# Optimization experiments

Measured on AMD Instinct MI355X. Metric: run time of the kernel, lower is better.

The kernel has to match this reference:

```python
import jax, jax.numpy as jnp
import numpy as np

N = 100000      # nodes
E = 1600000     # edges
NW = 512        # num_words (input feature dim)
H = 128         # hidden_size
L = 3           # num_layers
G = 256         # num graphs
NEG = 0.2       # GAT leaky_relu slope
EPS = 1e-5      # batchnorm eps


def setup_inputs() -> dict:
    key = jax.random.key(0)
    ks = jax.random.split(key, 20)
    x = jax.random.normal(ks[0], (N, NW), jnp.float32)
    edge_index = jax.random.randint(ks[1], (2, E), 0, N, dtype=jnp.int64)
    edge_attr = jax.random.randint(ks[2], (E,), 0, 8, dtype=jnp.int64)
    batch = jnp.sort(jax.random.randint(ks[3], (N,), 0, G, dtype=jnp.int64))
    edge_emb = jax.random.normal(ks[4], (8, H), jnp.float32) * 0.05
    W0 = jax.random.normal(ks[5], (NW, H), jnp.float32) / np.sqrt(NW)
    W_rest = jax.random.normal(ks[6], (L - 1, H, H), jnp.float32) / np.sqrt(H)
    att_src = jax.random.normal(ks[7], (L, H), jnp.float32) / np.sqrt(H)
    att_dst = jax.random.normal(ks[8], (L, H), jnp.float32) / np.sqrt(H)
    bias = jax.random.normal(ks[9], (L, H), jnp.float32) * 0.02
    gamma = 1.0 + jax.random.normal(ks[10], (L, H), jnp.float32) * 0.1
    beta = jax.random.normal(ks[11], (L, H), jnp.float32) * 0.02
    gate_w1 = jax.random.normal(ks[12], (H, H), jnp.float32) / np.sqrt(H)
    gate_b1 = jnp.zeros((H,), jnp.float32)
    gate_w2 = jax.random.normal(ks[13], (H, 1), jnp.float32) / np.sqrt(H)
    gate_b2 = jnp.zeros((1,), jnp.float32)
    cls_w = jax.random.normal(ks[14], (H, 2), jnp.float32) / np.sqrt(H)
    cls_b = jnp.zeros((2,), jnp.float32)
    return {"x": x, "edge_index": edge_index, "edge_attr": edge_attr, "batch": batch,
            "edge_emb": edge_emb, "W0": W0, "W_rest": W_rest, "att_src": att_src,
            "att_dst": att_dst, "bias": bias, "gamma": gamma, "beta": beta,
            "gate_w1": gate_w1, "gate_b1": gate_b1, "gate_w2": gate_w2,
            "gate_b2": gate_b2, "cls_w": cls_w, "cls_b": cls_b}


def _gat_layer(x, W, a_s, a_d, b, src, dst):
    # PyG GATConv, heads=1, concat=True: h = xW; e_ij = leaky(a_s.h_src + a_d.h_dst)
    h = x @ W                                   # [N, H]
    a_src = h @ a_s                             # [N]
    a_dst = h @ a_d                             # [N]
    e = jax.nn.leaky_relu(a_src[src] + a_dst[dst], NEG)      # [E+N]
    m = jax.ops.segment_max(e, dst, num_segments=N)          # scatter-softmax over dst
    ex = jnp.exp(e - m[dst])
    den = jax.ops.segment_sum(ex, dst, num_segments=N)
    coef = ex / den[dst]                                      # [E+N]
    out = jax.ops.segment_sum(h[src] * coef[:, None], dst, num_segments=N)
    return out + b


def _batchnorm_relu(x, g, bt):
    mu = jnp.mean(x, axis=0)
    var = jnp.mean((x - mu) ** 2, axis=0)      # biased variance (torch BN forward)
    return jax.nn.relu((x - mu) * jax.lax.rsqrt(var + EPS) * g + bt)


def reference(x, edge_index, edge_attr, batch, edge_emb, W0, W_rest, att_src,
              att_dst, bias, gamma, beta, gate_w1, gate_b1, gate_w2, gate_b2,
              cls_w, cls_b):
    _ = edge_emb[edge_attr]  # computed in original module but never used (DCE'd)
    # add self-loops as GATConv does by default
    loop = jnp.arange(N, dtype=edge_index.dtype)
    src = jnp.concatenate([edge_index[0], loop])
    dst = jnp.concatenate([edge_index[1], loop])
    Ws = [W0] + [W_rest[i] for i in range(L - 1)]
    for i in range(L):
        x = _gat_layer(x, Ws[i], att_src[i], att_dst[i], bias[i], src, dst)
        x = _batchnorm_relu(x, gamma[i], beta[i])  # dropout is identity in eval
    # GlobalAttention pooling: gate = MLP(x) -> segment softmax over graphs
    gate = jax.nn.relu(x @ gate_w1 + gate_b1) @ gate_w2 + gate_b2   # [N, 1]
    gate = gate[:, 0]
    gm = jax.ops.segment_max(gate, batch, num_segments=G)
    gex = jnp.exp(gate - gm[batch])
    gden = jax.ops.segment_sum(gex, batch, num_segments=G)
    gden = jnp.where(gden == 0, 1.0, gden)
    coef = gex / gden[batch]
    pooled = jax.ops.segment_sum(x * coef[:, None], batch, num_segments=G)  # [G, H]
    logits = pooled @ cls_w + cls_b
    return jax.nn.log_softmax(logits, axis=-1)
```

## Files before the change

kernel.cpp:

```cpp
#include <hip/hip_runtime.h>

#define kN  100000
#define kE  1600000
#define kNW 512
#define kH  128
#define kL  3
#define kG  256
#define kNEG 0.2f
#define kEPS 1e-5f

typedef __attribute__((ext_vector_type(8))) short bf16x8;
typedef __attribute__((ext_vector_type(4))) float f32x4;

static __device__ __forceinline__ float lrelu(float v) { return v >= 0.f ? v : kNEG * v; }

static __device__ __forceinline__ unsigned short bf16rn(float x) {
    unsigned u = __float_as_uint(x);
    return (unsigned short)((u + 0x7FFFu + ((u >> 16) & 1u)) >> 16);
}
static __device__ __forceinline__ float bf16tof(unsigned short h) {
    return __uint_as_float(((unsigned)h) << 16);
}

__global__ void count_deg(const int* __restrict__ ei, int* __restrict__ deg, int E) {
    int e = blockIdx.x * 256 + threadIdx.x;
    if (e < E) atomicAdd(&deg[ei[E + e]], 1);
}

__global__ void scan1(const int* __restrict__ deg, int* __restrict__ bsums, int n) {
    __shared__ int sdata[256];
    int b = blockIdx.x, t = threadIdx.x;
    int base = b * 1024 + t * 4;
    int s = 0;
#pragma unroll
    for (int j = 0; j < 4; j++) { int i = base + j; s += (i < n) ? deg[i] : 0; }
    sdata[t] = s; __syncthreads();
    for (int st = 128; st > 0; st >>= 1) { if (t < st) sdata[t] += sdata[t + st]; __syncthreads(); }
    if (t == 0) bsums[b] = sdata[0];
}

__global__ void scan2(int* __restrict__ bsums, int nb, int* __restrict__ row_ptr_last) {
    __shared__ int lds[128];
    int t = threadIdx.x;
    int v = (t < nb) ? bsums[t] : 0;
    lds[t] = v; __syncthreads();
    for (int st = 1; st < 128; st <<= 1) {
        int x = 0;
        if (t >= st) x = lds[t - st];
        __syncthreads();
        if (t >= st) lds[t] += x;
        __syncthreads();
    }
    if (t < nb) bsums[t] = lds[t] - v;
    if (t == nb - 1) row_ptr_last[0] = lds[t];
}

__global__ void scan3(const int* __restrict__ deg, const int* __restrict__ bsums,
                      int* __restrict__ row_ptr, int* __restrict__ cursor, int n) {
    __shared__ int lds[256];
    int b = blockIdx.x, t = threadIdx.x;
    int base = b * 1024 + t * 4;
    int v[4]; int s = 0;
#pragma unroll
    for (int j = 0; j < 4; j++) { int i = base + j; v[j] = (i < n) ? deg[i] : 0; s += v[j]; }
    lds[t] = s; __syncthreads();
    for (int st = 1; st < 256; st <<= 1) {
        int x = 0;
        if (t >= st) x = lds[t - st];
        __syncthreads();
        if (t >= st) lds[t] += x;
        __syncthreads();
    }
    int excl = (t == 0) ? 0 : lds[t - 1];
    excl += bsums[b];
    int run = excl;
#pragma unroll
    for (int j = 0; j < 4; j++) {
        int i = base + j;
        if (i < n) { row_ptr[i] = run; cursor[i] = run; run += v[j]; }
    }
}

__global__ void fill_csr(const int* __restrict__ ei, int* __restrict__ cursor,
                         int* __restrict__ col_src, int E) {
    int e = blockIdx.x * 256 + threadIdx.x;
    if (e < E) {
        int s = ei[e], d = ei[E + e];
        int p = atomicAdd(&cursor[d], 1);
        col_src[p] = s;
    }
}

__global__ void pack_a(const float* __restrict__ A, unsigned short* __restrict__ apk,
                       int Kpitch, int kbase, int NKT) {
    int g = blockIdx.x * 256 + threadIdx.x;
    int lane = g & 63;
    int t2 = g >> 6;
    int kt = t2 % NKT;
    int rt = t2 / NKT;
    int row = rt * 16 + (lane & 15);
    int k0 = kbase + kt * 32 + (lane >> 4) * 8;
    const float* src = A + (size_t)row * Kpitch + k0;
    float4 v0 = *(const float4*)src;
    float4 v1 = *(const float4*)(src + 4);
    float v[8] = {v0.x, v0.y, v0.z, v0.w, v1.x, v1.y, v1.z, v1.w};
    unsigned short h[8], l[8];
#pragma unroll
    for (int j = 0; j < 8; j++) {
        h[j] = bf16rn(v[j]);
        l[j] = bf16rn(v[j] - bf16tof(h[j]));
    }
    size_t slot = ((size_t)(rt * NKT + kt) * 2) * 512 + lane * 8;
    int4 vhi = make_int4((unsigned)h[0] | ((unsigned)h[1] << 16), (unsigned)h[2] | ((unsigned)h[3] << 16),
                         (unsigned)h[4] | ((unsigned)h[5] << 16), (unsigned)h[6] | ((unsigned)h[7] << 16));
    int4 vlo = make_int4((unsigned)l[0] | ((unsigned)l[1] << 16), (unsigned)l[2] | ((unsigned)l[3] << 16),
                         (unsigned)l[4] | ((unsigned)l[5] << 16), (unsigned)l[6] | ((unsigned)l[7] << 16));
    *(int4*)(apk + slot) = vhi;
    *(int4*)(apk + slot + 512) = vlo;
}

__global__ void pack_b_all(const float* __restrict__ W0, const float* __restrict__ Wr,
                           const float* __restrict__ Gw1,
                           unsigned short* __restrict__ b0a, unsigned short* __restrict__ b0b,
                           unsigned short* __restrict__ b1, unsigned short* __restrict__ b2,
                           unsigned short* __restrict__ bg) {
    int bid = blockIdx.x;
    const float* src; unsigned short* dst; int kbase; int NKT; int lb;
    if (bid < 16)      { src = W0;            dst = b0a; kbase = 0;   NKT = 8; lb = bid; }
    else if (bid < 32) { src = W0;            dst = b0b; kbase = 256; NKT = 8; lb = bid - 16; }
    else if (bid < 40) { src = Wr;            dst = b1;  kbase = 0;   NKT = 4; lb = bid - 32; }
    else if (bid < 48) { src = Wr + 128*128;  dst = b2;  kbase = 0;   NKT = 4; lb = bid - 40; }
    else               { src = Gw1;           dst = bg;  kbase = 0;   NKT = 4; lb = bid - 48; }
    int g = lb * 256 + threadIdx.x;
    int lane = g & 63;
    int t2 = g >> 6;
    int kt = t2 % NKT;
    int ct = t2 / NKT;
    int col = ct * 16 + (lane & 15);
    int k0 = kbase + kt * 32 + (lane >> 4) * 8;
    unsigned short h[8], l[8];
#pragma unroll
    for (int j = 0; j < 8; j++) {
        float v = src[(size_t)(k0 + j) * 128 + col];
        h[j] = bf16rn(v);
        l[j] = bf16rn(v - bf16tof(h[j]));
    }
    size_t slot = ((size_t)(ct * NKT + kt) * 2) * 512 + lane * 8;
    int4 vhi = make_int4((unsigned)h[0] | ((unsigned)h[1] << 16), (unsigned)h[2] | ((unsigned)h[3] << 16),
                         (unsigned)h[4] | ((unsigned)h[5] << 16), (unsigned)h[6] | ((unsigned)h[7] << 16));
    int4 vlo = make_int4((unsigned)l[0] | ((unsigned)l[1] << 16), (unsigned)l[2] | ((unsigned)l[3] << 16),
                         (unsigned)l[4] | ((unsigned)l[5] << 16), (unsigned)l[6] | ((unsigned)l[7] << 16));
    *(int4*)(dst + slot) = vhi;
    *(int4*)(dst + slot + 512) = vlo;
}

__global__ __launch_bounds__(256) void gemm_mfma(const unsigned short* __restrict__ apk,
                                                 const unsigned short* __restrict__ bpk,
                                                 float* __restrict__ C, int M, int NKT,
                                                 int accum, const float* __restrict__ bias,
                                                 int do_relu) {
    int tid = threadIdx.x;
    int w = tid >> 6, lane = tid & 63;
    int rt0 = blockIdx.x * 8 + (w >> 1) * 4;
    int ct0 = (w & 1) * 4;
    int laneoff = lane * 8;
    f32x4 acc[4][4];
#pragma unroll
    for (int i = 0; i < 4; i++)
#pragma unroll
        for (int j = 0; j < 4; j++) acc[i][j] = (f32x4){0.f, 0.f, 0.f, 0.f};

    for (int kt = 0; kt < NKT; ++kt) {
        bf16x8 Ah[4], Al[4], Bh[4], Bl[4];
#pragma unroll
        for (int f = 0; f < 4; f++) {
            size_t ao = ((size_t)((rt0 + f) * NKT + kt) * 2) * 512 + laneoff;
            Ah[f] = *(const bf16x8*)(apk + ao);
            Al[f] = *(const bf16x8*)(apk + ao + 512);
            size_t bo = ((size_t)((ct0 + f) * NKT + kt) * 2) * 512 + laneoff;
            Bh[f] = *(const bf16x8*)(bpk + bo);
            Bl[f] = *(const bf16x8*)(bpk + bo + 512);
        }
#pragma unroll
        for (int i = 0; i < 4; i++)
#pragma unroll
            for (int j = 0; j < 4; j++) {
                acc[i][j] = __builtin_amdgcn_mfma_f32_16x16x32_bf16(Ah[i], Bh[j], acc[i][j], 0, 0, 0);
                acc[i][j] = __builtin_amdgcn_mfma_f32_16x16x32_bf16(Ah[i], Bl[j], acc[i][j], 0, 0, 0);
                acc[i][j] = __builtin_amdgcn_mfma_f32_16x16x32_bf16(Al[i], Bh[j], acc[i][j], 0, 0, 0);
            }
    }
    int cbase = ct0 * 16 + (lane & 15);
    int rgrp = (lane >> 4) * 4;
#pragma unroll
    for (int i = 0; i < 4; i++) {
        int rbase = (rt0 + i) * 16 + rgrp;
#pragma unroll
        for (int j = 0; j < 4; j++) {
            int col = cbase + j * 16;
#pragma unroll
            for (int r = 0; r < 4; r++) {
                int row = rbase + r;
                if (row < M) {
                    float v = acc[i][j][r];
                    if (accum) v += C[(size_t)row * 128 + col];
                    if (bias) v += bias[col];
                    if (do_relu) v = fmaxf(v, 0.f);
                    C[(size_t)row * 128 + col] = v;
                }
            }
        }
    }
}

__global__ void att_dots(const float* __restrict__ h, const float* __restrict__ ws_,
                         const float* __restrict__ wd_, float* __restrict__ a_s,
                         float* __restrict__ a_d, int n) {
    int v = blockIdx.x * 4 + (threadIdx.x >> 6);
    int lane = threadIdx.x & 63;
    if (v >= n) return;
    float2 hx = ((const float2*)(h + (size_t)v * 128))[lane];
    float2 ws = ((const float2*)ws_)[lane];
    float2 wd = ((const float2*)wd_)[lane];
    float ps = hx.x * ws.x + hx.y * ws.y;
    float pd = hx.x * wd.x + hx.y * wd.y;
#pragma unroll
    for (int off = 32; off; off >>= 1) {
        ps += __shfl_xor(ps, off);
        pd += __shfl_xor(pd, off);
    }
    if (lane == 0) { a_s[v] = ps; a_d[v] = pd; }
}

__global__ void edge_softmax(const int* __restrict__ row_ptr, const int* __restrict__ col_src,
                             const float* __restrict__ a_s, const float* __restrict__ a_d,
                             float* __restrict__ coef, float* __restrict__ coef_self, int n) {
    int v = blockIdx.x * 4 + (threadIdx.x >> 6);
    int lane = threadIdx.x & 63;
    if (v >= n) return;
    int s0 = row_ptr[v], s1 = row_ptr[v + 1];
    float adv = a_d[v];
    float es = lrelu(a_s[v] + adv);
    float mx = es;
    for (int k = s0 + lane; k < s1; k += 64) {
        float e = lrelu(a_s[col_src[k]] + adv);
        coef[k] = e;
        mx = fmaxf(mx, e);
    }
#pragma unroll
    for (int off = 32; off; off >>= 1) mx = fmaxf(mx, __shfl_xor(mx, off));
    float sum = 0.f;
    for (int k = s0 + lane; k < s1; k += 64) {
        float ex = expf(coef[k] - mx);
        coef[k] = ex;
        sum += ex;
    }
    if (lane == 0) sum += expf(es - mx);
#pragma unroll
    for (int off = 32; off; off >>= 1) sum += __shfl_xor(sum, off);
    float inv = 1.f / sum;
    for (int k = s0 + lane; k < s1; k += 64) coef[k] *= inv;
    if (lane == 0) coef_self[v] = expf(es - mx) * inv;
}

__global__ void aggregate(const int* __restrict__ row_ptr, const int* __restrict__ col_src,
                          const float* __restrict__ coef, const float* __restrict__ coef_self,
                          const float* __restrict__ h, const float* __restrict__ bias,
                          float* __restrict__ out, int n) {
    int v = blockIdx.x * 4 + (threadIdx.x >> 6);
    int lane = threadIdx.x & 63;
    if (v >= n) return;
    int s0 = row_ptr[v], s1 = row_ptr[v + 1];
    const float2* h2 = (const float2*)h;
    float cs = coef_self[v];
    float2 hv = h2[(size_t)v * 64 + lane];
    float ax = cs * hv.x, ay = cs * hv.y;
    for (int k = s0; k < s1; k++) {
        int s = col_src[k];
        float c = coef[k];
        float2 hs = h2[(size_t)s * 64 + lane];
        ax += c * hs.x;
        ay += c * hs.y;
    }
    float2 b = ((const float2*)bias)[lane];
    float2 o; o.x = ax + b.x; o.y = ay + b.y;
    ((float2*)out)[(size_t)v * 64 + lane] = o;
}

__global__ void bn_stats(const float* __restrict__ x, double* __restrict__ sums, int n) {
    int col = threadIdx.x & 127;
    int half = threadIdx.x >> 7;
    double s = 0.0, q = 0.0;
    for (int r = blockIdx.x * 2 + half; r < n; r += gridDim.x * 2) {
        float v = x[(size_t)r * 128 + col];
        s += v;
        q += (double)v * (double)v;
    }
    __shared__ double ls[256], lq[256];
    ls[threadIdx.x] = s; lq[threadIdx.x] = q;
    __syncthreads();
    if (half == 0) {
        s += ls[threadIdx.x + 128];
        q += lq[threadIdx.x + 128];
        atomicAdd(&sums[col], s);
        atomicAdd(&sums[128 + col], q);
    }
}

__global__ void bn_finalize(const double* __restrict__ sums, const float* __restrict__ gamma,
                            const float* __restrict__ beta, float* __restrict__ coefs, int n) {
    int c = threadIdx.x;
    if (c < 128) {
        double mu = sums[c] / n;
        double var = sums[128 + c] / n - mu * mu;
        double rs = 1.0 / sqrt(var + (double)kEPS);
        float sc = (float)rs * gamma[c];
        coefs[c] = sc;
        coefs[128 + c] = beta[c] - (float)(mu * rs) * gamma[c];
    }
}

__global__ void bn_apply_pack(const float* __restrict__ xin, const float* __restrict__ coefs,
                              unsigned short* __restrict__ apk, float* __restrict__ xout, int n) {
    int idx = blockIdx.x * 256 + threadIdx.x;
    if (idx >= n * 32) return;
    float4 v = ((const float4*)xin)[idx];
    int c4 = idx & 31;
    int r = idx >> 5;
    int c = c4 * 4;
    v.x = fmaxf(v.x * coefs[c + 0] + coefs[128 + c + 0], 0.f);
    v.y = fmaxf(v.y * coefs[c + 1] + coefs[128 + c + 1], 0.f);
    v.z = fmaxf(v.z * coefs[c + 2] + coefs[128 + c + 2], 0.f);
    v.w = fmaxf(v.w * coefs[c + 3] + coefs[128 + c + 3], 0.f);
    if (xout) ((float4*)xout)[idx] = v;
    int rt = r >> 4;
    int kt = c >> 5;
    int lane = (r & 15) + (((c >> 3) & 3) << 4);
    int half = c4 & 1;
    size_t slot = ((size_t)(rt * 4 + kt) * 2) * 512 + lane * 8 + half * 4;
    float vv[4] = {v.x, v.y, v.z, v.w};
    unsigned short h[4], l[4];
#pragma unroll
    for (int j = 0; j < 4; j++) {
        h[j] = bf16rn(vv[j]);
        l[j] = bf16rn(vv[j] - bf16tof(h[j]));
    }
    int2 vhi = make_int2((unsigned)h[0] | ((unsigned)h[1] << 16), (unsigned)h[2] | ((unsigned)h[3] << 16));
    int2 vlo = make_int2((unsigned)l[0] | ((unsigned)l[1] << 16), (unsigned)l[2] | ((unsigned)l[3] << 16));
    *(int2*)(apk + slot) = vhi;
    *(int2*)(apk + slot + 512) = vlo;
}

__global__ void gate_dot(const float* __restrict__ hidden, const float* __restrict__ gw2,
                         const float* __restrict__ gb2, float* __restrict__ gate, int n) {
    int v = blockIdx.x * 4 + (threadIdx.x >> 6);
    int lane = threadIdx.x & 63;
    if (v >= n) return;
    float2 hx = ((const float2*)(hidden + (size_t)v * 128))[lane];
    float2 w = ((const float2*)gw2)[lane];
    float p = hx.x * w.x + hx.y * w.y;
#pragma unroll
    for (int off = 32; off; off >>= 1) p += __shfl_xor(p, off);
    if (lane == 0) gate[v] = p + gb2[0];
}

__global__ void graph_bounds(const int* __restrict__ batch, int* __restrict__ gstart, int n, int g) {
    int i = blockIdx.x * 256 + threadIdx.x;
    if (i > g) return;
    int lo = 0, hi = n;
    while (lo < hi) {
        int mid = (lo + hi) >> 1;
        if (batch[mid] < i) lo = mid + 1; else hi = mid;
    }
    gstart[i] = lo;
}

__global__ __launch_bounds__(512) void pool(const float* __restrict__ x, const float* __restrict__ gate,
                                            const int* __restrict__ gstart, float* __restrict__ pooled) {
    int g = blockIdx.x;
    int t = threadIdx.x;
    int col = t & 127;
    int q = t >> 7;
    int s0 = gstart[g], s1 = gstart[g + 1];
    __shared__ float red[8];
    __shared__ float acc_lds[512];
    float mx = -INFINITY;
    for (int v = s0 + t; v < s1; v += 512) mx = fmaxf(mx, gate[v]);
#pragma unroll
    for (int off = 32; off; off >>= 1) mx = fmaxf(mx, __shfl_xor(mx, off));
    if ((t & 63) == 0) red[t >> 6] = mx;
    __syncthreads();
    mx = fmaxf(fmaxf(fmaxf(red[0], red[1]), fmaxf(red[2], red[3])),
               fmaxf(fmaxf(red[4], red[5]), fmaxf(red[6], red[7])));
    __syncthreads();
    float sum = 0.f;
    for (int v = s0 + t; v < s1; v += 512) sum += expf(gate[v] - mx);
#pragma unroll
    for (int off = 32; off; off >>= 1) sum += __shfl_xor(sum, off);
    if ((t & 63) == 0) red[t >> 6] = sum;
    __syncthreads();
    sum = red[0] + red[1] + red[2] + red[3] + red[4] + red[5] + red[6] + red[7];
    if (sum == 0.f) sum = 1.f;
    float inv = 1.f / sum;
    float acc = 0.f;
    for (int v = s0 + q; v < s1; v += 4) {
        float c = expf(gate[v] - mx) * inv;
        acc += x[(size_t)v * 128 + col] * c;
    }
    acc_lds[t] = acc;
    __syncthreads();
    if (q == 0)
        pooled[(size_t)g * 128 + col] = acc_lds[col] + acc_lds[128 + col] +
                                        acc_lds[256 + col] + acc_lds[384 + col];
}

__global__ void classify(const float* __restrict__ pooled, const float* __restrict__ cls_w,
                         const float* __restrict__ cls_b, float* __restrict__ out, int g_) {
    int g = blockIdx.x * 4 + (threadIdx.x >> 6);
    int lane = threadIdx.x & 63;
    if (g >= g_) return;
    float2 p = ((const float2*)(pooled + (size_t)g * 128))[lane];
    float4 w = ((const float4*)cls_w)[lane];
    float l0 = p.x * w.x + p.y * w.z;
    float l1 = p.x * w.y + p.y * w.w;
#pragma unroll
    for (int off = 32; off; off >>= 1) {
        l0 += __shfl_xor(l0, off);
        l1 += __shfl_xor(l1, off);
    }
    if (lane == 0) {
        l0 += cls_b[0]; l1 += cls_b[1];
        float m = fmaxf(l0, l1);
        float lse = m + logf(expf(l0 - m) + expf(l1 - m));
        out[g * 2 + 0] = l0 - lse;
        out[g * 2 + 1] = l1 - lse;
    }
}

extern "C" void kernel_launch(void* const* d_in, const int* in_sizes, int n_in,
                              void* d_out, int out_size, void* d_ws, size_t ws_size,
                              hipStream_t stream) {
    const float* x        = (const float*)d_in[0];
    const int*   ei       = (const int*)d_in[1];
    const int*   batch    = (const int*)d_in[3];
    const float* W0       = (const float*)d_in[5];
    const float* W_rest   = (const float*)d_in[6];
    const float* att_src  = (const float*)d_in[7];
    const float* att_dst  = (const float*)d_in[8];
    const float* bias     = (const float*)d_in[9];
    const float* gamma    = (const float*)d_in[10];
    const float* beta     = (const float*)d_in[11];
    const float* gate_w1  = (const float*)d_in[12];
    const float* gate_b1  = (const float*)d_in[13];
    const float* gate_w2  = (const float*)d_in[14];
    const float* gate_b2  = (const float*)d_in[15];
    const float* cls_w    = (const float*)d_in[16];
    const float* cls_b    = (const float*)d_in[17];
    float* out = (float*)d_out;

    char* ws = (char*)d_ws;
    size_t off = 0;
    auto take = [&](size_t bytes) -> void* {
        void* p = ws + off;
        off += (bytes + 255) & ~(size_t)255;
        return p;
    };
    const int NRT = 6256;
    float* h         = (float*)take((size_t)kN * kH * 4);
    float* xa        = (float*)take((size_t)kN * kH * 4);
    unsigned short* apk = (unsigned short*)take((size_t)NRT * 8 * 2 * 512 * 2);
    unsigned short* bpk0a = (unsigned short*)take(8 * 8 * 2 * 512 * 2);
    unsigned short* bpk0b = (unsigned short*)take(8 * 8 * 2 * 512 * 2);
    unsigned short* bpk1  = (unsigned short*)take(8 * 4 * 2 * 512 * 2);
    unsigned short* bpk2  = (unsigned short*)take(8 * 4 * 2 * 512 * 2);
    unsigned short* bpkg  = (unsigned short*)take(8 * 4 * 2 * 512 * 2);
    float* a_s       = (float*)take((size_t)kN * 4);
    float* a_d       = (float*)take((size_t)kN * 4);
    float* coef_self = (float*)take((size_t)kN * 4);
    int*   deg       = (int*)take((size_t)kN * 4);
    int*   cursor    = (int*)take((size_t)kN * 4);
    int*   row_ptr   = (int*)take((size_t)(kN + 1) * 4);
    int*   col_src   = (int*)take((size_t)kE * 4);
    float* coef_csr  = (float*)take((size_t)kE * 4);
    int*   bsums     = (int*)take(1024 * 4);
    double* bn_sums  = (double*)take(256 * 8);
    float* bn_coefs  = (float*)take(256 * 4);
    float* gate      = (float*)take((size_t)kN * 4);
    int*   gstart    = (int*)take((size_t)(kG + 1) * 4);
    float* pooled    = (float*)take((size_t)kG * kH * 4);
    (void)ws_size; (void)in_sizes; (void)n_in; (void)out_size;

    const int NB = (kN + 1023) / 1024;
    const int GEMM_BLKS = (kN + 127) / 128;

    hipMemsetAsync(deg, 0, (size_t)kN * 4, stream);
    count_deg<<<(kE + 255) / 256, 256, 0, stream>>>(ei, deg, kE);
    scan1<<<NB, 256, 0, stream>>>(deg, bsums, kN);
    scan2<<<1, 128, 0, stream>>>(bsums, NB, row_ptr + kN);
    scan3<<<NB, 256, 0, stream>>>(deg, bsums, row_ptr, cursor, kN);
    fill_csr<<<(kE + 255) / 256, 256, 0, stream>>>(ei, cursor, col_src, kE);

    pack_b_all<<<56, 256, 0, stream>>>(W0, W_rest, gate_w1, bpk0a, bpk0b, bpk1, bpk2, bpkg);

    pack_a<<<6250 * 8 / 4, 256, 0, stream>>>(x, apk, kNW, 0, 8);
    gemm_mfma<<<GEMM_BLKS, 256, 0, stream>>>(apk, bpk0a, h, kN, 8, 0, nullptr, 0);
    pack_a<<<6250 * 8 / 4, 256, 0, stream>>>(x, apk, kNW, 256, 8);
    gemm_mfma<<<GEMM_BLKS, 256, 0, stream>>>(apk, bpk0b, h, kN, 8, 1, nullptr, 0);

    for (int l = 0; l < kL; l++) {
        if (l > 0) {
            const unsigned short* bp = (l == 1) ? bpk1 : bpk2;
            gemm_mfma<<<GEMM_BLKS, 256, 0, stream>>>(apk, bp, h, kN, 4, 0, nullptr, 0);
        }
        att_dots<<<(kN + 3) / 4, 256, 0, stream>>>(h, att_src + (size_t)l * kH,
                                                   att_dst + (size_t)l * kH, a_s, a_d, kN);
        edge_softmax<<<(kN + 3) / 4, 256, 0, stream>>>(row_ptr, col_src, a_s, a_d,
                                                       coef_csr, coef_self, kN);
        aggregate<<<(kN + 3) / 4, 256, 0, stream>>>(row_ptr, col_src, coef_csr, coef_self,
                                                    h, bias + (size_t)l * kH, xa, kN);
        hipMemsetAsync(bn_sums, 0, 256 * 8, stream);
        bn_stats<<<1024, 256, 0, stream>>>(xa, bn_sums, kN);
        bn_finalize<<<1, 128, 0, stream>>>(bn_sums, gamma + (size_t)l * kH,
                                           beta + (size_t)l * kH, bn_coefs, kN);
        bn_apply_pack<<<((kN * 32) + 255) / 256, 256, 0, stream>>>(
            xa, bn_coefs, apk, (l == kL - 1) ? xa : nullptr, kN);
    }

    gemm_mfma<<<GEMM_BLKS, 256, 0, stream>>>(apk, bpkg, h, kN, 4, 0, gate_b1, 1);
    gate_dot<<<(kN + 3) / 4, 256, 0, stream>>>(h, gate_w2, gate_b2, gate, kN);

    graph_bounds<<<2, 256, 0, stream>>>(batch, gstart, kN, kG);
    pool<<<kG, 512, 0, stream>>>(xa, gate, gstart, pooled);
    classify<<<(kG + 3) / 4, 256, 0, stream>>>(pooled, cls_w, cls_b, out, kG);
}
```

Measured before the change: 1.613 ms.

## Fuse packing, batchnorm-apply and attention dots into GEMM; fuse edge softmax with aggregation

The GEMM now reads fp32 activations directly and splits them into bf16 hi/lo inside the kernel. It applies the previous layer's batchnorm+ReLU in its prologue and computes the attention (or gate) dot products in its epilogue. This removes the separate pack_a, bn_apply_pack, att_dots and gate_dot passes and their intermediate buffers. Edge softmax and neighbor aggregation are merged into one kernel that builds exp weights on the fly, avoiding the E-sized coefficient array, and bn_stats is vectorized. The trade-off is heavier GEMM kernels with redundant per-tile conversion, possible register pressure, and dropping gate_b2, which relies on softmax shift invariance.

```diff
diff --git a/kernel.cpp b/kernel.cpp
--- a/kernel.cpp
+++ b/kernel.cpp
@@ -91,53 +91,23 @@
     }
 }
 
-__global__ void pack_a(const float* __restrict__ A, unsigned short* __restrict__ apk,
-                       int Kpitch, int kbase, int NKT) {
-    int g = blockIdx.x * 256 + threadIdx.x;
-    int lane = g & 63;
-    int t2 = g >> 6;
-    int kt = t2 % NKT;
-    int rt = t2 / NKT;
-    int row = rt * 16 + (lane & 15);
-    int k0 = kbase + kt * 32 + (lane >> 4) * 8;
-    const float* src = A + (size_t)row * Kpitch + k0;
-    float4 v0 = *(const float4*)src;
-    float4 v1 = *(const float4*)(src + 4);
-    float v[8] = {v0.x, v0.y, v0.z, v0.w, v1.x, v1.y, v1.z, v1.w};
-    unsigned short h[8], l[8];
-#pragma unroll
-    for (int j = 0; j < 8; j++) {
-        h[j] = bf16rn(v[j]);
-        l[j] = bf16rn(v[j] - bf16tof(h[j]));
-    }
-    size_t slot = ((size_t)(rt * NKT + kt) * 2) * 512 + lane * 8;
-    int4 vhi = make_int4((unsigned)h[0] | ((unsigned)h[1] << 16), (unsigned)h[2] | ((unsigned)h[3] << 16),
-                         (unsigned)h[4] | ((unsigned)h[5] << 16), (unsigned)h[6] | ((unsigned)h[7] << 16));
-    int4 vlo = make_int4((unsigned)l[0] | ((unsigned)l[1] << 16), (unsigned)l[2] | ((unsigned)l[3] << 16),
-                         (unsigned)l[4] | ((unsigned)l[5] << 16), (unsigned)l[6] | ((unsigned)l[7] << 16));
-    *(int4*)(apk + slot) = vhi;
-    *(int4*)(apk + slot + 512) = vlo;
-}
-
 __global__ void pack_b_all(const float* __restrict__ W0, const float* __restrict__ Wr,
                            const float* __restrict__ Gw1,
-                           unsigned short* __restrict__ b0a, unsigned short* __restrict__ b0b,
-                           unsigned short* __restrict__ b1, unsigned short* __restrict__ b2,
-                           unsigned short* __restrict__ bg) {
+                           unsigned short* __restrict__ b0, unsigned short* __restrict__ b1,
+                           unsigned short* __restrict__ b2, unsigned short* __restrict__ bg) {
     int bid = blockIdx.x;
-    const float* src; unsigned short* dst; int kbase; int NKT; int lb;
-    if (bid < 16)      { src = W0;            dst = b0a; kbase = 0;   NKT = 8; lb = bid; }
-    else if (bid < 32) { src = W0;            dst = b0b; kbase = 256; NKT = 8; lb = bid - 16; }
-    else if (bid < 40) { src = Wr;            dst = b1;  kbase = 0;   NKT = 4; lb = bid - 32; }
-    else if (bid < 48) { src = Wr + 128*128;  dst = b2;  kbase = 0;   NKT = 4; lb = bid - 40; }
-    else               { src = Gw1;           dst = bg;  kbase = 0;   NKT = 4; lb = bid - 48; }
+    const float* src; unsigned short* dst; int NKT; int lb;
+    if (bid < 32)      { src = W0;            dst = b0; NKT = 16; lb = bid; }
+    else if (bid < 40) { src = Wr;            dst = b1; NKT = 4;  lb = bid - 32; }
+    else if (bid < 48) { src = Wr + 128*128;  dst = b2; NKT = 4;  lb = bid - 40; }
+    else               { src = Gw1;           dst = bg; NKT = 4;  lb = bid - 48; }
     int g = lb * 256 + threadIdx.x;
     int lane = g & 63;
     int t2 = g >> 6;
     int kt = t2 % NKT;
     int ct = t2 / NKT;
     int col = ct * 16 + (lane & 15);
-    int k0 = kbase + kt * 32 + (lane >> 4) * 8;
+    int k0 = kt * 32 + (lane >> 4) * 8;
     unsigned short h[8], l[8];
 #pragma unroll
     for (int j = 0; j < 8; j++) {
@@ -154,16 +124,28 @@
     *(int4*)(dst + slot + 512) = vlo;
 }
 
-__global__ __launch_bounds__(256) void gemm_mfma(const unsigned short* __restrict__ apk,
-                                                 const unsigned short* __restrict__ bpk,
-                                                 float* __restrict__ C, int M, int NKT,
-                                                 int accum, const float* __restrict__ bias,
-                                                 int do_relu) {
+__global__ __launch_bounds__(256) void gemm_cvt(const float* __restrict__ A, int Kpitch, int NKT,
+                                                const unsigned short* __restrict__ bpk,
+                                                float* __restrict__ C, int M,
+                                                const float* __restrict__ bias, int do_relu,
+                                                const float* __restrict__ abn,
+                                                const float* __restrict__ att_s,
+                                                const float* __restrict__ att_d,
+                                                float* __restrict__ a_s, float* __restrict__ a_d) {
+    __shared__ float sAs[4][64], sAd[4][64];
     int tid = threadIdx.x;
     int w = tid >> 6, lane = tid & 63;
     int rt0 = blockIdx.x * 8 + (w >> 1) * 4;
     int ct0 = (w & 1) * 4;
     int laneoff = lane * 8;
+    int ksub = (lane >> 4) * 8;
+    const float* arow[4];
+#pragma unroll
+    for (int f = 0; f < 4; f++) {
+        int row = (rt0 + f) * 16 + (lane & 15);
+        if (row > M - 1) row = M - 1;
+        arow[f] = A + (size_t)row * Kpitch;
+    }
     f32x4 acc[4][4];
 #pragma unroll
     for (int i = 0; i < 4; i++)
@@ -171,12 +153,32 @@
         for (int j = 0; j < 4; j++) acc[i][j] = (f32x4){0.f, 0.f, 0.f, 0.f};
 
     for (int kt = 0; kt < NKT; ++kt) {
+        int k0 = kt * 32 + ksub;
+        float sc[8], sh[8];
+        if (abn) {
+            float4 s0 = *(const float4*)(abn + k0);
+            float4 s1 = *(const float4*)(abn + k0 + 4);
+            float4 t0 = *(const float4*)(abn + 128 + k0);
+            float4 t1 = *(const float4*)(abn + 128 + k0 + 4);
+            sc[0]=s0.x; sc[1]=s0.y; sc[2]=s0.z; sc[3]=s0.w;
+            sc[4]=s1.x; sc[5]=s1.y; sc[6]=s1.z; sc[7]=s1.w;
+            sh[0]=t0.x; sh[1]=t0.y; sh[2]=t0.z; sh[3]=t0.w;
+            sh[4]=t1.x; sh[5]=t1.y; sh[6]=t1.z; sh[7]=t1.w;
+        }
         bf16x8 Ah[4], Al[4], Bh[4], Bl[4];
 #pragma unroll
         for (int f = 0; f < 4; f++) {
-            size_t ao = ((size_t)((rt0 + f) * NKT + kt) * 2) * 512 + laneoff;
-            Ah[f] = *(const bf16x8*)(apk + ao);
-            Al[f] = *(const bf16x8*)(apk + ao + 512);
+            float4 v0 = *(const float4*)(arow[f] + k0);
+            float4 v1 = *(const float4*)(arow[f] + k0 + 4);
+            float v[8] = {v0.x, v0.y, v0.z, v0.w, v1.x, v1.y, v1.z, v1.w};
+#pragma unroll
+            for (int j = 0; j < 8; j++) {
+                float vj = v[j];
+                if (abn) vj = fmaxf(vj * sc[j] + sh[j], 0.f);
+                unsigned short hh = bf16rn(vj);
+                Ah[f][j] = (short)hh;
+                Al[f][j] = (short)bf16rn(vj - bf16tof(hh));
+            }
             size_t bo = ((size_t)((ct0 + f) * NKT + kt) * 2) * 512 + laneoff;
             Bh[f] = *(const bf16x8*)(bpk + bo);
             Bl[f] = *(const bf16x8*)(bpk + bo + 512);
@@ -192,122 +194,174 @@
     }
     int cbase = ct0 * 16 + (lane & 15);
     int rgrp = (lane >> 4) * 4;
+    float atts[4], attd[4];
+    if (att_s) {
+#pragma unroll
+        for (int j = 0; j < 4; j++) { atts[j] = att_s[cbase + j * 16]; attd[j] = att_d[cbase + j * 16]; }
+    }
+    float asp[4][4], adp[4][4];
 #pragma unroll
     for (int i = 0; i < 4; i++) {
         int rbase = (rt0 + i) * 16 + rgrp;
 #pragma unroll
+        for (int r = 0; r < 4; r++) { asp[i][r] = 0.f; adp[i][r] = 0.f; }
+#pragma unroll
         for (int j = 0; j < 4; j++) {
             int col = cbase + j * 16;
 #pragma unroll
             for (int r = 0; r < 4; r++) {
+                float val = acc[i][j][r];
+                if (bias) val += bias[col];
+                if (do_relu) val = fmaxf(val, 0.f);
                 int row = rbase + r;
-                if (row < M) {
-                    float v = acc[i][j][r];
-                    if (accum) v += C[(size_t)row * 128 + col];
-                    if (bias) v += bias[col];
-                    if (do_relu) v = fmaxf(v, 0.f);
-                    C[(size_t)row * 128 + col] = v;
+                if (C && row < M) C[(size_t)row * 128 + col] = val;
+                if (att_s) { asp[i][r] += val * atts[j]; adp[i][r] += val * attd[j]; }
+            }
+        }
+    }
+    if (att_s) {
+#pragma unroll
+        for (int i = 0; i < 4; i++)
+#pragma unroll
+            for (int r = 0; r < 4; r++) {
+                float s = asp[i][r], d = adp[i][r];
+#pragma unroll
+                for (int off = 1; off < 16; off <<= 1) {
+                    s += __shfl_xor(s, off);
+                    d += __shfl_xor(d, off);
+                }
+                if ((lane & 15) == 0) {
+                    int rl = i * 16 + rgrp + r;
+                    sAs[w][rl] = s; sAd[w][rl] = d;
                 }
             }
+        __syncthreads();
+        if (tid < 128) {
+            int grow = blockIdx.x * 128 + tid;
+            if (grow < M) {
+                int wp = (tid >> 6) * 2, rl = tid & 63;
+                a_s[grow] = sAs[wp][rl] + sAs[wp + 1][rl];
+                if (a_d) a_d[grow] = sAd[wp][rl] + sAd[wp + 1][rl];
+            }
         }
     }
 }
 
-__global__ void att_dots(const float* __restrict__ h, const float* __restrict__ ws_,
-                         const float* __restrict__ wd_, float* __restrict__ a_s,
-                         float* __restrict__ a_d, int n) {
-    int v = blockIdx.x * 4 + (threadIdx.x >> 6);
-    int lane = threadIdx.x & 63;
-    if (v >= n) return;
-    float2 hx = ((const float2*)(h + (size_t)v * 128))[lane];
-    float2 ws = ((const float2*)ws_)[lane];
-    float2 wd = ((const float2*)wd_)[lane];
-    float ps = hx.x * ws.x + hx.y * ws.y;
-    float pd = hx.x * wd.x + hx.y * wd.y;
-#pragma unroll
-    for (int off = 32; off; off >>= 1) {
-        ps += __shfl_xor(ps, off);
-        pd += __shfl_xor(pd, off);
-    }
-    if (lane == 0) { a_s[v] = ps; a_d[v] = pd; }
-}
-
-__global__ void edge_softmax(const int* __restrict__ row_ptr, const int* __restrict__ col_src,
-                             const float* __restrict__ a_s, const float* __restrict__ a_d,
-                             float* __restrict__ coef, float* __restrict__ coef_self, int n) {
+static __device__ __forceinline__ void gather_chunk(const float2* __restrict__ h2, int lane,
+                                                    int s_l, float ex_l, int cnt,
+                                                    float& ax, float& ay) {
+    for (int e0 = 0; e0 < cnt; e0 += 8) {
+        int t0 = __shfl(s_l, e0 + 0); float c0 = __shfl(ex_l, e0 + 0);
+        int t1 = __shfl(s_l, e0 + 1); float c1 = __shfl(ex_l, e0 + 1);
+        int t2 = __shfl(s_l, e0 + 2); float c2 = __shfl(ex_l, e0 + 2);
+        int t3 = __shfl(s_l, e0 + 3); float c3 = __shfl(ex_l, e0 + 3);
+        int t4 = __shfl(s_l, e0 + 4); float c4 = __shfl(ex_l, e0 + 4);
+        int t5 = __shfl(s_l, e0 + 5); float c5 = __shfl(ex_l, e0 + 5);
+        int t6 = __shfl(s_l, e0 + 6); float c6 = __shfl(ex_l, e0 + 6);
+        int t7 = __shfl(s_l, e0 + 7); float c7 = __shfl(ex_l, e0 + 7);
+        float2 h0 = h2[(size_t)t0 * 64 + lane];
+        float2 h1 = h2[(size_t)t1 * 64 + lane];
+        float2 h2v = h2[(size_t)t2 * 64 + lane];
+        float2 h3 = h2[(size_t)t3 * 64 + lane];
+        float2 h4 = h2[(size_t)t4 * 64 + lane];
+        float2 h5 = h2[(size_t)t5 * 64 + lane];
+        float2 h6 = h2[(size_t)t6 * 64 + lane];
+        float2 h7 = h2[(size_t)t7 * 64 + lane];
+        ax += c0 * h0.x + c1 * h1.x + c2 * h2v.x + c3 * h3.x
+            + c4 * h4.x + c5 * h5.x + c6 * h6.x + c7 * h7.x;
+        ay += c0 * h0.y + c1 * h1.y + c2 * h2v.y + c3 * h3.y
+            + c4 * h4.y + c5 * h5.y + c6 * h6.y + c7 * h7.y;
+    }
+}
+
+__global__ __launch_bounds__(256) void gat_edge(const int* __restrict__ row_ptr,
+                                                const int* __restrict__ col_src,
+                                                const float* __restrict__ a_s,
+                                                const float* __restrict__ a_d,
+                                                const float* __restrict__ h,
+                                                const float* __restrict__ bias,
+                                                float* __restrict__ out, int n) {
     int v = blockIdx.x * 4 + (threadIdx.x >> 6);
     int lane = threadIdx.x & 63;
     if (v >= n) return;
     int s0 = row_ptr[v], s1 = row_ptr[v + 1];
     float adv = a_d[v];
-    float es = lrelu(a_s[v] + adv);
-    float mx = es;
-    for (int k = s0 + lane; k < s1; k += 64) {
-        float e = lrelu(a_s[col_src[k]] + adv);
-        coef[k] = e;
-        mx = fmaxf(mx, e);
-    }
+    float e_self = lrelu(a_s[v] + adv);
+    int idx0 = s0 + lane;
+    bool act0 = idx0 < s1;
+    int sl0 = act0 ? col_src[idx0] : 0;
+    float el0 = act0 ? lrelu(a_s[sl0] + adv) : -1e30f;
+    float mx = fmaxf(e_self, el0);
+    for (int k = s0 + 64 + lane; k < s1; k += 64)
+        mx = fmaxf(mx, lrelu(a_s[col_src[k]] + adv));
 #pragma unroll
     for (int off = 32; off; off >>= 1) mx = fmaxf(mx, __shfl_xor(mx, off));
-    float sum = 0.f;
-    for (int k = s0 + lane; k < s1; k += 64) {
-        float ex = expf(coef[k] - mx);
-        coef[k] = ex;
-        sum += ex;
-    }
-    if (lane == 0) sum += expf(es - mx);
-#pragma unroll
-    for (int off = 32; off; off >>= 1) sum += __shfl_xor(sum, off);
-    float inv = 1.f / sum;
-    for (int k = s0 + lane; k < s1; k += 64) coef[k] *= inv;
-    if (lane == 0) coef_self[v] = expf(es - mx) * inv;
-}
-
-__global__ void aggregate(const int* __restrict__ row_ptr, const int* __restrict__ col_src,
-                          const float* __restrict__ coef, const float* __restrict__ coef_self,
-                          const float* __restrict__ h, const float* __restrict__ bias,
-                          float* __restrict__ out, int n) {
-    int v = blockIdx.x * 4 + (threadIdx.x >> 6);
-    int lane = threadIdx.x & 63;
-    if (v >= n) return;
-    int s0 = row_ptr[v], s1 = row_ptr[v + 1];
+
     const float2* h2 = (const float2*)h;
-    float cs = coef_self[v];
+    float ax = 0.f, ay = 0.f, den = 0.f;
+    {
+        float exl = act0 ? __expf(el0 - mx) : 0.f;
+        den += exl;
+        int cnt = s1 - s0; if (cnt > 64) cnt = 64;
+        gather_chunk(h2, lane, sl0, exl, cnt, ax, ay);
+    }
+    for (int k0 = s0 + 64; k0 < s1; k0 += 64) {
+        int idx = k0 + lane;
+        bool act = idx < s1;
+        int s_l = act ? col_src[idx] : 0;
+        float exl = act ? __expf(lrelu(a_s[s_l] + adv) - mx) : 0.f;
+        den += exl;
+        int cnt = s1 - k0; if (cnt > 64) cnt = 64;
+        gather_chunk(h2, lane, s_l, exl, cnt, ax, ay);
+    }
+#pragma unroll
+    for (int off = 32; off; off >>= 1) den += __shfl_xor(den, off);
+    float es = __expf(e_self - mx);
+    den += es;
     float2 hv = h2[(size_t)v * 64 + lane];
-    float ax = cs * hv.x, ay = cs * hv.y;
-    for (int k = s0; k < s1; k++) {
-        int s = col_src[k];
-        float c = coef[k];
-        float2 hs = h2[(size_t)s * 64 + lane];
-        ax += c * hs.x;
-        ay += c * hs.y;
-    }
+    ax += es * hv.x; ay += es * hv.y;
+    float inv = 1.f / den;
     float2 b = ((const float2*)bias)[lane];
-    float2 o; o.x = ax + b.x; o.y = ay + b.y;
+    float2 o; o.x = ax * inv + b.x; o.y = ay * inv + b.y;
     ((float2*)out)[(size_t)v * 64 + lane] = o;
 }
 
-__global__ void bn_stats(const float* __restrict__ x, double* __restrict__ sums, int n) {
-    int col = threadIdx.x & 127;
-    int half = threadIdx.x >> 7;
-    double s = 0.0, q = 0.0;
-    for (int r = blockIdx.x * 2 + half; r < n; r += gridDim.x * 2) {
-        float v = x[(size_t)r * 128 + col];
-        s += v;
-        q += (double)v * (double)v;
-    }
-    __shared__ double ls[256], lq[256];
-    ls[threadIdx.x] = s; lq[threadIdx.x] = q;
+__global__ __launch_bounds__(256) void bn_stats(const float* __restrict__ x,
+                                                double* __restrict__ sums, int n) {
+    int c4 = (threadIdx.x & 31) * 4;
+    int rg = threadIdx.x >> 5;
+    double s0 = 0, s1 = 0, s2 = 0, s3 = 0, q0 = 0, q1 = 0, q2 = 0, q3 = 0;
+    for (int r = blockIdx.x * 8 + rg; r < n; r += gridDim.x * 8) {
+        float4 v = *(const float4*)(x + (size_t)r * 128 + c4);
+        s0 += v.x; q0 += (double)v.x * v.x;
+        s1 += v.y; q1 += (double)v.y * v.y;
+        s2 += v.z; q2 += (double)v.z * v.z;
+        s3 += v.w; q3 += (double)v.w * v.w;
+    }
+    __shared__ double ls[8][128], lq[8][128];
+    ls[rg][c4] = s0; ls[rg][c4 + 1] = s1; ls[rg][c4 + 2] = s2; ls[rg][c4 + 3] = s3;
+    lq[rg][c4] = q0; lq[rg][c4 + 1] = q1; lq[rg][c4 + 2] = q2; lq[rg][c4 + 3] = q3;
     __syncthreads();
-    if (half == 0) {
-        s += ls[threadIdx.x + 128];
-        q += lq[threadIdx.x + 128];
-        atomicAdd(&sums[col], s);
-        atomicAdd(&sums[128 + col], q);
-    }
-}
-
-__global__ void bn_finalize(const double* __restrict__ sums, const float* __restrict__ gamma,
+    for (int st = 4; st > 0; st >>= 1) {
+        if (rg < st) {
+#pragma unroll
+            for (int j = 0; j < 4; j++) {
+                ls[rg][c4 + j] += ls[rg + st][c4 + j];
+                lq[rg][c4 + j] += lq[rg + st][c4 + j];
+            }
+        }
+        __syncthreads();
+    }
+    if (rg == 0) {
+#pragma unroll
+        for (int j = 0; j < 4; j++) {
+            atomicAdd(&sums[c4 + j], ls[0][c4 + j]);
+            atomicAdd(&sums[128 + c4 + j], lq[0][c4 + j]);
+        }
+    }
+}
+
+__global__ void bn_finalize(double* __restrict__ sums, const float* __restrict__ gamma,
                             const float* __restrict__ beta, float* __restrict__ coefs, int n) {
     int c = threadIdx.x;
     if (c < 128) {
@@ -317,51 +371,9 @@
         float sc = (float)rs * gamma[c];
         coefs[c] = sc;
         coefs[128 + c] = beta[c] - (float)(mu * rs) * gamma[c];
-    }
-}
-
-__global__ void bn_apply_pack(const float* __restrict__ xin, const float* __restrict__ coefs,
-                              unsigned short* __restrict__ apk, float* __restrict__ xout, int n) {
-    int idx = blockIdx.x * 256 + threadIdx.x;
-    if (idx >= n * 32) return;
-    float4 v = ((const float4*)xin)[idx];
-    int c4 = idx & 31;
-    int r = idx >> 5;
-    int c = c4 * 4;
-    v.x = fmaxf(v.x * coefs[c + 0] + coefs[128 + c + 0], 0.f);
-    v.y = fmaxf(v.y * coefs[c + 1] + coefs[128 + c + 1], 0.f);
-    v.z = fmaxf(v.z * coefs[c + 2] + coefs[128 + c + 2], 0.f);
-    v.w = fmaxf(v.w * coefs[c + 3] + coefs[128 + c + 3], 0.f);
-    if (xout) ((float4*)xout)[idx] = v;
-    int rt = r >> 4;
-    int kt = c >> 5;
-    int lane = (r & 15) + (((c >> 3) & 3) << 4);
-    int half = c4 & 1;
-    size_t slot = ((size_t)(rt * 4 + kt) * 2) * 512 + lane * 8 + half * 4;
-    float vv[4] = {v.x, v.y, v.z, v.w};
-    unsigned short h[4], l[4];
-#pragma unroll
-    for (int j = 0; j < 4; j++) {
-        h[j] = bf16rn(vv[j]);
-        l[j] = bf16rn(vv[j] - bf16tof(h[j]));
-    }
-    int2 vhi = make_int2((unsigned)h[0] | ((unsigned)h[1] << 16), (unsigned)h[2] | ((unsigned)h[3] << 16));
-    int2 vlo = make_int2((unsigned)l[0] | ((unsigned)l[1] << 16), (unsigned)l[2] | ((unsigned)l[3] << 16));
-    *(int2*)(apk + slot) = vhi;
-    *(int2*)(apk + slot + 512) = vlo;
-}
-
-__global__ void gate_dot(const float* __restrict__ hidden, const float* __restrict__ gw2,
-                         const float* __restrict__ gb2, float* __restrict__ gate, int n) {
-    int v = blockIdx.x * 4 + (threadIdx.x >> 6);
-    int lane = threadIdx.x & 63;
-    if (v >= n) return;
-    float2 hx = ((const float2*)(hidden + (size_t)v * 128))[lane];
-    float2 w = ((const float2*)gw2)[lane];
-    float p = hx.x * w.x + hx.y * w.y;
-#pragma unroll
-    for (int off = 32; off; off >>= 1) p += __shfl_xor(p, off);
-    if (lane == 0) gate[v] = p + gb2[0];
+        sums[c] = 0.0;
+        sums[128 + c] = 0.0;
+    }
 }
 
 __global__ void graph_bounds(const int* __restrict__ batch, int* __restrict__ gstart, int n, int g) {
@@ -376,12 +388,15 @@
 }
 
 __global__ __launch_bounds__(512) void pool(const float* __restrict__ x, const float* __restrict__ gate,
-                                            const int* __restrict__ gstart, float* __restrict__ pooled) {
+                                            const int* __restrict__ gstart,
+                                            const float* __restrict__ abn,
+                                            float* __restrict__ pooled) {
     int g = blockIdx.x;
     int t = threadIdx.x;
     int col = t & 127;
     int q = t >> 7;
     int s0 = gstart[g], s1 = gstart[g + 1];
+    float scale = abn[col], shift = abn[128 + col];
     __shared__ float red[8];
     __shared__ float acc_lds[512];
     float mx = -INFINITY;
@@ -405,7 +420,8 @@
     float acc = 0.f;
     for (int v = s0 + q; v < s1; v += 4) {
         float c = expf(gate[v] - mx) * inv;
-        acc += x[(size_t)v * 128 + col] * c;
+        float xv = fmaxf(x[(size_t)v * 128 + col] * scale + shift, 0.f);
+        acc += xv * c;
     }
     acc_lds[t] = acc;
     __syncthreads();
@@ -453,7 +469,6 @@
     const float* gate_w1  = (const float*)d_in[12];
     const float* gate_b1  = (const float*)d_in[13];
     const float* gate_w2  = (const float*)d_in[14];
-    const float* gate_b2  = (const float*)d_in[15];
     const float* cls_w    = (const float*)d_in[16];
     const float* cls_b    = (const float*)d_in[17];
     float* out = (float*)d_out;
@@ -465,23 +480,18 @@
         off += (bytes + 255) & ~(size_t)255;
         return p;
     };
-    const int NRT = 6256;
     float* h         = (float*)take((size_t)kN * kH * 4);
     float* xa        = (float*)take((size_t)kN * kH * 4);
-    unsigned short* apk = (unsigned short*)take((size_t)NRT * 8 * 2 * 512 * 2);
-    unsigned short* bpk0a = (unsigned short*)take(8 * 8 * 2 * 512 * 2);
-    unsigned short* bpk0b = (unsigned short*)take(8 * 8 * 2 * 512 * 2);
-    unsigned short* bpk1  = (unsigned short*)take(8 * 4 * 2 * 512 * 2);
-    unsigned short* bpk2  = (unsigned short*)take(8 * 4 * 2 * 512 * 2);
-    unsigned short* bpkg  = (unsigned short*)take(8 * 4 * 2 * 512 * 2);
+    unsigned short* bpk0 = (unsigned short*)take(8 * 16 * 2 * 512 * 2);
+    unsigned short* bpk1 = (unsigned short*)take(8 * 4 * 2 * 512 * 2);
+    unsigned short* bpk2 = (unsigned short*)take(8 * 4 * 2 * 512 * 2);
+    unsigned short* bpkg = (unsigned short*)take(8 * 4 * 2 * 512 * 2);
     float* a_s       = (float*)take((size_t)kN * 4);
     float* a_d       = (float*)take((size_t)kN * 4);
-    float* coef_self = (float*)take((size_t)kN * 4);
     int*   deg       = (int*)take((size_t)kN * 4);
     int*   cursor    = (int*)take((size_t)kN * 4);
     int*   row_ptr   = (int*)take((size_t)(kN + 1) * 4);
     int*   col_src   = (int*)take((size_t)kE * 4);
-    float* coef_csr  = (float*)take((size_t)kE * 4);
     int*   bsums     = (int*)take(1024 * 4);
     double* bn_sums  = (double*)take(256 * 8);
     float* bn_coefs  = (float*)take(256 * 4);
@@ -494,42 +504,35 @@
     const int GEMM_BLKS = (kN + 127) / 128;
 
     hipMemsetAsync(deg, 0, (size_t)kN * 4, stream);
+    hipMemsetAsync(bn_sums, 0, 256 * 8, stream);
     count_deg<<<(kE + 255) / 256, 256, 0, stream>>>(ei, deg, kE);
     scan1<<<NB, 256, 0, stream>>>(deg, bsums, kN);
     scan2<<<1, 128, 0, stream>>>(bsums, NB, row_ptr + kN);
     scan3<<<NB, 256, 0, stream>>>(deg, bsums, row_ptr, cursor, kN);
     fill_csr<<<(kE + 255) / 256, 256, 0, stream>>>(ei, cursor, col_src, kE);
 
-    pack_b_all<<<56, 256, 0, stream>>>(W0, W_rest, gate_w1, bpk0a, bpk0b, bpk1, bpk2, bpkg);
-
-    pack_a<<<6250 * 8 / 4, 256, 0, stream>>>(x, apk, kNW, 0, 8);
-    gemm_mfma<<<GEMM_BLKS, 256, 0, stream>>>(apk, bpk0a, h, kN, 8, 0, nullptr, 0);
-    pack_a<<<6250 * 8 / 4, 256, 0, stream>>>(x, apk, kNW, 256, 8);
-    gemm_mfma<<<GEMM_BLKS, 256, 0, stream>>>(apk, bpk0b, h, kN, 8, 1, nullptr, 0);
+    pack_b_all<<<56, 256, 0, stream>>>(W0, W_rest, gate_w1, bpk0, bpk1, bpk2, bpkg);
 
     for (int l = 0; l < kL; l++) {
-        if (l > 0) {
-            const unsigned short* bp = (l == 1) ? bpk1 : bpk2;
-            gemm_mfma<<<GEMM_BLKS, 256, 0, stream>>>(apk, bp, h, kN, 4, 0, nullptr, 0);
-        }
-        att_dots<<<(kN + 3) / 4, 256, 0, stream>>>(h, att_src + (size_t)l * kH,
-                                                   att_dst + (size_t)l * kH, a_s, a_d, kN);
-        edge_softmax<<<(kN + 3) / 4, 256, 0, stream>>>(row_ptr, col_src, a_s, a_d,
-                                                       coef_csr, coef_self, kN);
-        aggregate<<<(kN + 3) / 4, 256, 0, stream>>>(row_ptr, col_src, coef_csr, coef_self,
-                                                    h, bias + (size_t)l * kH, xa, kN);
-        hipMemsetAsync(bn_sums, 0, 256 * 8, stream);
+        const float* Ain = (l == 0) ? x : xa;
+        int Kp = (l == 0) ? kNW : kH;
+        int NKT = (l == 0) ? 16 : 4;
+        const unsigned short* bp = (l == 0) ? bpk0 : ((l == 1) ? bpk1 : bpk2);
+        const float* abn = (l == 0) ? nullptr : bn_coefs;
+        gemm_cvt<<<GEMM_BLKS, 256, 0, stream>>>(Ain, Kp, NKT, bp, h, kN, nullptr, 0, abn,
+                                                att_src + (size_t)l * kH, att_dst + (size_t)l * kH,
+                                                a_s, a_d);
+        gat_edge<<<(kN + 3) / 4, 256, 0, stream>>>(row_ptr, col_src, a_s, a_d, h,
+                                                   bias + (size_t)l * kH, xa, kN);
         bn_stats<<<1024, 256, 0, stream>>>(xa, bn_sums, kN);
         bn_finalize<<<1, 128, 0, stream>>>(bn_sums, gamma + (size_t)l * kH,
                                            beta + (size_t)l * kH, bn_coefs, kN);
-        bn_apply_pack<<<((kN * 32) + 255) / 256, 256, 0, stream>>>(
-            xa, bn_coefs, apk, (l == kL - 1) ? xa : nullptr, kN);
-    }
-
-    gemm_mfma<<<GEMM_BLKS, 256, 0, stream>>>(apk, bpkg, h, kN, 4, 0, gate_b1, 1);
-    gate_dot<<<(kN + 3) / 4, 256, 0, stream>>>(h, gate_w2, gate_b2, gate, kN);
+    }
+
+    gemm_cvt<<<GEMM_BLKS, 256, 0, stream>>>(xa, kH, 4, bpkg, nullptr, kN, gate_b1, 1,
+                                            bn_coefs, gate_w2, gate_w2, gate, nullptr);
 
     graph_bounds<<<2, 256, 0, stream>>>(batch, gstart, kN, kG);
-    pool<<<kG, 512, 0, stream>>>(xa, gate, gstart, pooled);
+    pool<<<kG, 512, 0, stream>>>(xa, gate, gstart, bn_coefs, pooled);
     classify<<<(kG + 3) / 4, 256, 0, stream>>>(pooled, cls_w, cls_b, out, kG);
 }
```

Result: faster. 1.382 ms (-14.3%).
